# Optimization experiments

Hardware: AMD Instinct MI355X
Metric: run time of the kernel (lower is better)

Reference implementation:

```python
import jax, jax.numpy as jnp
import numpy as np

N = 50000       # nodes
E = 800000      # edges (before self-loops)
G = 512         # graphs in batch
IN_DIM = 128
OUT_DIM = 8
DIMS = [(IN_DIM, 32), (32, 64), (64, 128), (128, 64)]
EPS = 1e-5


def setup_inputs() -> dict:
    key = jax.random.key(0)
    ks = jax.random.split(key, 40)
    def nrm(k, shape, s=0.05):
        return jax.random.normal(k, shape, jnp.float32) * s
    inp = {}
    inp["x"] = jax.random.normal(ks[0], (N, IN_DIM), jnp.float32)
    inp["edge_index"] = jax.random.randint(ks[1], (2, E), 0, N, dtype=jnp.int32)
    inp["batch"] = jnp.sort(jax.random.randint(ks[2], (N,), 0, G, dtype=jnp.int32))
    for i, (din, dout) in enumerate(DIMS, 1):
        inp[f"W{i}"]  = nrm(ks[3 * i + 0], (din, dout))
        inp[f"as{i}"] = nrm(ks[3 * i + 1], (dout,))
        inp[f"ad{i}"] = nrm(ks[3 * i + 2], (dout,))
        inp[f"b{i}"]  = jnp.zeros((dout,), jnp.float32)
        inp[f"g{i}"]  = jnp.ones((dout,), jnp.float32)   # BN gamma
        inp[f"be{i}"] = jnp.zeros((dout,), jnp.float32)  # BN beta
    inp["Wf"] = nrm(ks[20], (64, 32)); inp["bf"] = jnp.zeros((32,), jnp.float32)
    inp["Wc"] = nrm(ks[21], (32, OUT_DIM)); inp["bc"] = jnp.zeros((OUT_DIM,), jnp.float32)
    return inp


def gat_conv(x, src, dst, W, a_s, a_d, b):
    """PyG GATConv, heads=1: linear (no bias) -> per-edge attention with
    leaky_relu(0.2) -> segment softmax over incoming edges -> scatter-add -> bias."""
    h = x @ W                                   # [N, F]
    a_src = h @ a_s                             # [N]
    a_dst = h @ a_d                             # [N]
    e = jax.nn.leaky_relu(a_src[src] + a_dst[dst], 0.2)   # [E+N]
    m = jax.ops.segment_max(e, dst, num_segments=N)
    w = jnp.exp(e - m[dst])
    denom = jax.ops.segment_sum(w, dst, num_segments=N)
    alpha = w / denom[dst]                      # self-loops guarantee denom > 0
    out = jax.ops.segment_sum(alpha[:, None] * h[src], dst, num_segments=N)
    return out + b


def batch_norm(x, g, be):
    mu = x.mean(axis=0)
    var = x.var(axis=0)                         # biased, as torch training BN
    return (x - mu) * jax.lax.rsqrt(var + EPS) * g + be


def reference(x, edge_index, batch,
              W1, as1, ad1, b1, g1, be1,
              W2, as2, ad2, b2, g2, be2,
              W3, as3, ad3, b3, g3, be3,
              W4, as4, ad4, b4, g4, be4,
              Wf, bf, Wc, bc):
    loops = jnp.arange(N, dtype=edge_index.dtype)
    src = jnp.concatenate([edge_index[0], loops])   # GATConv adds self-loops
    dst = jnp.concatenate([edge_index[1], loops])
    params = [(W1, as1, ad1, b1, g1, be1), (W2, as2, ad2, b2, g2, be2),
              (W3, as3, ad3, b3, g3, be3), (W4, as4, ad4, b4, g4, be4)]
    h = x
    for (W, a_s, a_d, b, g, be) in params:
        h = jax.nn.leaky_relu(gat_conv(h, src, dst, W, a_s, a_d, b), 0.01)
        h = batch_norm(h, g, be)
    pooled = jax.ops.segment_sum(h, batch, num_segments=G)   # global_add_pool
    z = jax.nn.leaky_relu(pooled @ Wf + bf, 0.01)
    return jax.nn.sigmoid(z @ Wc + bc)
```

## Files before the change

### kernel.cpp

```cpp
#include <hip/hip_runtime.h>
#include <math.h>

constexpr int BLK = 256;
constexpr int NBLKA = 256;

static inline int cdiv(long a, long b) { return (int)((a + b - 1) / b); }

typedef __attribute__((ext_vector_type(8))) short short8;
typedef __attribute__((ext_vector_type(4))) float floatx4;

__device__ __forceinline__ unsigned short f2bf(float f) {
    unsigned u = __float_as_uint(f);
    unsigned r = u + 0x7fffu + ((u >> 16) & 1u);
    return (unsigned short)(r >> 16);
}
__device__ __forceinline__ float bf2f(unsigned short s) {
    return __uint_as_float(((unsigned)s) << 16);
}


__global__ void histA_k(const int* __restrict__ dst, int* __restrict__ histg,
                        int E, int nbkt, int chunk) {
    __shared__ int h[256];
    int tid = threadIdx.x, z = blockIdx.x;
    h[tid] = 0;
    __syncthreads();
    int e0 = z * chunk, e1 = min(E, e0 + chunk);
    for (int e = e0 + tid; e < e1; e += BLK) atomicAdd(&h[dst[e] >> 8], 1);
    __syncthreads();
    if (tid < nbkt) histg[z * nbkt + tid] = h[tid];
}

__global__ void bucket_scan_k(const int* __restrict__ histg, int* __restrict__ bucket_base,
                              int nbkt, int E, int* __restrict__ gs, int* __restrict__ ge,
                              int G, float* __restrict__ bnstats) {
    __shared__ int s[BLK];
    int t = threadIdx.x;
    int v = 0;
    if (t < nbkt)
        for (int z = 0; z < NBLKA; ++z) v += histg[z * nbkt + t];
    s[t] = v;
    __syncthreads();
    for (int o = 1; o < BLK; o <<= 1) {
        int tv = (t >= o) ? s[t - o] : 0;
        __syncthreads();
        s[t] += tv;
        __syncthreads();
    }
    if (t < nbkt) bucket_base[t] = s[t] - v;
    if (t == 0) bucket_base[nbkt] = E;
    for (int i = t; i < G; i += BLK) { gs[i] = 0x7fffffff; ge[i] = -1; }
    for (int i = t; i < 1024; i += BLK) bnstats[i] = 0.f;
}

__global__ void blk_scan_k(int* __restrict__ histg, const int* __restrict__ bucket_base,
                           int nbkt) {
    __shared__ int s[BLK];
    int t = threadIdx.x, b = blockIdx.x;
    int v = histg[t * nbkt + b];
    s[t] = v;
    __syncthreads();
    for (int o = 1; o < BLK; o <<= 1) {
        int tv = (t >= o) ? s[t - o] : 0;
        __syncthreads();
        s[t] += tv;
        __syncthreads();
    }
    histg[t * nbkt + b] = bucket_base[b] + s[t] - v;
}

__global__ void scatterA_k(const int* __restrict__ src, const int* __restrict__ dst,
                           const int* __restrict__ histg, unsigned* __restrict__ ebkt,
                           int E, int nbkt, int chunk) {
    __shared__ int cur[256];
    int tid = threadIdx.x, z = blockIdx.x;
    if (tid < nbkt) cur[tid] = histg[z * nbkt + tid];
    __syncthreads();
    int e0 = z * chunk, e1 = min(E, e0 + chunk);
    for (int e = e0 + tid; e < e1; e += BLK) {
        int d = dst[e];
        int b = d >> 8;
        int pos = atomicAdd(&cur[b], 1);
        ebkt[pos] = ((unsigned)(d & 255) << 16) | (unsigned)src[e];
    }
}

__global__ void csrB_k(const unsigned* __restrict__ ebkt, const int* __restrict__ bucket_base,
                       int* __restrict__ off, unsigned short* __restrict__ csr,
                       const int* __restrict__ batch, int* __restrict__ gs,
                       int* __restrict__ ge, int N, int E, int nbkt) {
    __shared__ int dg[256];
    __shared__ int sc[256];
    int t = threadIdx.x, b = blockIdx.x;
    int n0 = b << 8;
    int cnt = min(256, N - n0);
    dg[t] = (t < cnt) ? 1 : 0;
    __syncthreads();
    int e0 = bucket_base[b], e1 = bucket_base[b + 1];
    for (int e = e0 + t; e < e1; e += BLK) atomicAdd(&dg[ebkt[e] >> 16], 1);
    __syncthreads();
    int d = dg[t];
    sc[t] = d;
    __syncthreads();
    for (int o = 1; o < BLK; o <<= 1) {
        int tv = (t >= o) ? sc[t - o] : 0;
        __syncthreads();
        sc[t] += tv;
        __syncthreads();
    }
    int loff = sc[t] - d;
    int csrbase = e0 + n0;
    if (t < cnt) {
        off[n0 + t] = csrbase + loff;
        csr[csrbase + loff] = (unsigned short)(n0 + t);
        dg[t] = loff + 1;
    }
    if (b == nbkt - 1 && t == 0) off[N] = E + N;
    int n = n0 + t;
    if (n < N) {
        int bb = batch[n];
        if (n == 0) gs[bb] = 0;
        else {
            int pb = batch[n - 1];
            if (pb != bb) { gs[bb] = n; ge[pb] = n - 1; }
        }
        if (n == N - 1) ge[bb] = N - 1;
    }
    __syncthreads();
    for (int e = e0 + t; e < e1; e += BLK) {
        unsigned w = ebkt[e];
        int pos = atomicAdd(&dg[w >> 16], 1);
        csr[csrbase + pos] = (unsigned short)(w & 0xffff);
    }
}

template <int K, int NOUT, bool AFP32, bool HASBN>
__launch_bounds__(256)
__global__ void gemm_fused(const void* __restrict__ av, const float* __restrict__ W,
                           const float* __restrict__ a_s, const float* __restrict__ a_d,
                           const float* __restrict__ bnst, const float* __restrict__ g_prev,
                           const float* __restrict__ be_prev, float invN,
                           unsigned short* __restrict__ hb,
                           float* __restrict__ asrc, float* __restrict__ adst, int N) {
    constexpr int KF = K / 32;
    __shared__ float s_sca[K], s_scc[K], s_rs[K], s_rd[K], s_bd[2];
    int tid = threadIdx.x;
    if (tid < K) {
        float a = 1.f, c = 0.f;
        if (HASBN) {
            float mu = bnst[tid] * invN;
            float var = bnst[128 + tid] * invN - mu * mu;
            a = g_prev[tid] * rsqrtf(var + 1e-5f);
            c = be_prev[tid] - mu * a;
        }
        s_sca[tid] = a; s_scc[tid] = c;
    }
    __syncthreads();
    const bool dots = (blockIdx.y == 0);
    if (dots) {
        if (tid < K) {
            const float* wr = W + (long)tid * NOUT;
            float rs = 0.f, rd = 0.f;
            for (int f = 0; f < NOUT; ++f) {
                float w = wr[f];
                rs += w * a_s[f];
                rd += w * a_d[f];
            }
            s_rs[tid] = rs; s_rd[tid] = rd;
        }
        __syncthreads();
        if (tid < 2) {
            const float* r = tid ? s_rd : s_rs;
            float b = 0.f;
            for (int k = 0; k < K; ++k) b += s_scc[k] * r[k];
            s_bd[tid] = b;
        }
        __syncthreads();
    }

    int wave = tid >> 6;
    int lane = tid & 63;
    int quad = lane >> 4;
    int r16 = lane & 15;
    int col = blockIdx.y * 16 + r16;

    short8 bfr[KF];
    float biasp = 0.f;
#pragma unroll
    for (int kk = 0; kk < KF; ++kk) {
        short8 b;
#pragma unroll
        for (int j = 0; j < 8; ++j) {
            int k = kk * 32 + quad * 8 + j;
            float w = W[(long)k * NOUT + col];
            b[j] = (short)f2bf(s_sca[k] * w);
            biasp += s_scc[k] * w;
        }
        bfr[kk] = b;
    }
    biasp += __shfl_xor(biasp, 16, 64);
    biasp += __shfl_xor(biasp, 32, 64);

    int blockbase = blockIdx.x * 128;
#pragma unroll
    for (int rt = 0; rt < 2; ++rt) {
        int tilebase = blockbase + wave * 32 + rt * 16;
        if (tilebase >= N) break;
        int arow = min(tilebase + r16, N - 1);
        short8 afr[KF];
        if (AFP32) {
            const float* xr = (const float*)av + (long)arow * K;
#pragma unroll
            for (int kk = 0; kk < KF; ++kk) {
                float4 x0 = *(const float4*)(xr + kk * 32 + quad * 8);
                float4 x1 = *(const float4*)(xr + kk * 32 + quad * 8 + 4);
                short8 a;
                a[0] = (short)f2bf(x0.x); a[1] = (short)f2bf(x0.y);
                a[2] = (short)f2bf(x0.z); a[3] = (short)f2bf(x0.w);
                a[4] = (short)f2bf(x1.x); a[5] = (short)f2bf(x1.y);
                a[6] = (short)f2bf(x1.z); a[7] = (short)f2bf(x1.w);
                afr[kk] = a;
            }
        } else {
            const unsigned short* hr = (const unsigned short*)av + (long)arow * K;
#pragma unroll
            for (int kk = 0; kk < KF; ++kk)
                afr[kk] = *(const short8*)(hr + kk * 32 + quad * 8);
        }
        floatx4 acc = {0.f, 0.f, 0.f, 0.f};
#pragma unroll
        for (int kk = 0; kk < KF; ++kk)
            acc = __builtin_amdgcn_mfma_f32_16x16x32_bf16(afr[kk], bfr[kk], acc, 0, 0, 0);
#pragma unroll
        for (int rr = 0; rr < 4; ++rr) {
            int srow = tilebase + quad * 4 + rr;
            if (srow < N) hb[(long)srow * NOUT + col] = f2bf(acc[rr] + biasp);
        }
        if (dots) {
            float ds = 0.f, dd = 0.f;
#pragma unroll
            for (int kk = 0; kk < KF; ++kk) {
                int kb = kk * 32 + quad * 8;
#pragma unroll
                for (int j = 0; j < 8; ++j) {
                    int k = kb + j;
                    float a = bf2f((unsigned short)afr[kk][j]) * s_sca[k];
                    ds += a * s_rs[k];
                    dd += a * s_rd[k];
                }
            }
            ds += __shfl_xor(ds, 16, 64); ds += __shfl_xor(ds, 32, 64);
            dd += __shfl_xor(dd, 16, 64); dd += __shfl_xor(dd, 32, 64);
            int drow = tilebase + r16;
            if (quad == 0 && drow < N) {
                asrc[drow] = ds + s_bd[0];
                adst[drow] = dd + s_bd[1];
            }
        }
    }
}

template <int DOUT>
__global__ void gather_fused(const int* __restrict__ off,
                             const unsigned short* __restrict__ csr,
                             const float* __restrict__ asrc, const float* __restrict__ adst,
                             const unsigned short* __restrict__ hb,
                             const float* __restrict__ b,
                             unsigned short* __restrict__ out, int N) {
    constexpr int TPN = DOUT / 8;
    int t = blockIdx.x * blockDim.x + threadIdx.x;
    int d = t / TPN;
    if (d >= N) return;
    int l = t % TPN;
    int p0 = off[d], p1 = off[d + 1];
    float ad = adst[d];
    const int f0 = l * 8;

    float acc[8];
#pragma unroll
    for (int i = 0; i < 8; ++i) acc[i] = 0.f;
    float sum = 0.f;

#pragma unroll 2
    for (int p = p0; p < p1; ++p) {
        int s = csr[p];
        float e = asrc[s] + ad;
        e = e > 0.f ? e : 0.2f * e;
        float w = __expf(e);
        sum += w;
        const uint4 hv = *(const uint4*)(hb + (long)s * DOUT + f0);
        acc[0] += w * bf2f((unsigned short)(hv.x & 0xffff));
        acc[1] += w * bf2f((unsigned short)(hv.x >> 16));
        acc[2] += w * bf2f((unsigned short)(hv.y & 0xffff));
        acc[3] += w * bf2f((unsigned short)(hv.y >> 16));
        acc[4] += w * bf2f((unsigned short)(hv.z & 0xffff));
        acc[5] += w * bf2f((unsigned short)(hv.z >> 16));
        acc[6] += w * bf2f((unsigned short)(hv.w & 0xffff));
        acc[7] += w * bf2f((unsigned short)(hv.w >> 16));
    }
    float inv = 1.f / sum;

    float4 b0 = *(const float4*)(b + f0);
    float4 b1 = *(const float4*)(b + f0 + 4);
    float bb[8] = {b0.x, b0.y, b0.z, b0.w, b1.x, b1.y, b1.z, b1.w};
    ushort4 o0, o1;
#pragma unroll
    for (int i = 0; i < 8; ++i) {
        float v = acc[i] * inv + bb[i];
        v = v > 0.f ? v : 0.01f * v;
        unsigned short hv = f2bf(v);
        if (i < 4) ((unsigned short*)&o0)[i] = hv;
        else       ((unsigned short*)&o1)[i - 4] = hv;
    }
    *(ushort4*)(out + (long)d * DOUT + f0) = o0;
    *(ushort4*)(out + (long)d * DOUT + f0 + 4) = o1;
}

template <int DOUT>
__global__ void stats_k(const unsigned short* __restrict__ y, float* __restrict__ bnsum,
                        float* __restrict__ bnsq, int N) {
    constexpr int QPR = DOUT / 8;
    __shared__ float ssum[DOUT];
    __shared__ float ssq[DOUT];
    for (int i = threadIdx.x; i < DOUT; i += blockDim.x) { ssum[i] = 0.f; ssq[i] = 0.f; }
    __syncthreads();
    long total = (long)N * QPR;
    long stride = (long)gridDim.x * blockDim.x;
    long t0 = (long)blockIdx.x * blockDim.x + threadIdx.x;
    int f0 = (int)(t0 % QPR) * 8;
    float ls[8], lq[8];
#pragma unroll
    for (int i = 0; i < 8; ++i) { ls[i] = 0.f; lq[i] = 0.f; }
    for (long t = t0; t < total; t += stride) {
        uint4 hv = *(const uint4*)(y + t * 8);
        unsigned vv[4] = {hv.x, hv.y, hv.z, hv.w};
#pragma unroll
        for (int q = 0; q < 4; ++q) {
            float v0 = bf2f((unsigned short)(vv[q] & 0xffff));
            float v1 = bf2f((unsigned short)(vv[q] >> 16));
            ls[2 * q] += v0;     lq[2 * q] += v0 * v0;
            ls[2 * q + 1] += v1; lq[2 * q + 1] += v1 * v1;
        }
    }
#pragma unroll
    for (int i = 0; i < 8; ++i) {
        atomicAdd(&ssum[f0 + i], ls[i]);
        atomicAdd(&ssq[f0 + i], lq[i]);
    }
    __syncthreads();
    for (int i = threadIdx.x; i < DOUT; i += blockDim.x) {
        atomicAdd(&bnsum[i], ssum[i]);
        atomicAdd(&bnsq[i], ssq[i]);
    }
}

__global__ void pool_head_k(const unsigned short* __restrict__ h, const int* __restrict__ gs,
                            const int* __restrict__ ge, const float* __restrict__ bnst,
                            const float* __restrict__ g4, const float* __restrict__ be4,
                            float invN, const float* __restrict__ Wf,
                            const float* __restrict__ bf, const float* __restrict__ Wc,
                            const float* __restrict__ bc, float* __restrict__ out) {
    int g = blockIdx.x;
    int t = threadIdx.x;
    __shared__ float p[64];
    __shared__ float z[32];
    float mu = bnst[t] * invN;
    float var = bnst[128 + t] * invN - mu * mu;
    float a = g4[t] * rsqrtf(var + 1e-5f);
    float c = be4[t] - mu * a;
    int s0 = gs[g], s1 = ge[g];
    float acc = 0.f, cnt = 0.f;
    if (s0 <= s1) {
        cnt = (float)(s1 - s0 + 1);
        for (int n = s0; n <= s1; ++n) acc += bf2f(h[(long)n * 64 + t]);
    }
    p[t] = a * acc + cnt * c;
    __syncthreads();
    if (t < 32) {
        float zacc = bf[t];
#pragma unroll
        for (int f = 0; f < 64; ++f) zacc += p[f] * Wf[f * 32 + t];
        z[t] = zacc > 0.f ? zacc : 0.01f * zacc;
    }
    __syncthreads();
    if (t < 8) {
        float oacc = bc[t];
#pragma unroll
        for (int o = 0; o < 32; ++o) oacc += z[o] * Wc[o * 8 + t];
        out[(long)g * 8 + t] = 1.f / (1.f + __expf(-oacc));
    }
}

extern "C" void kernel_launch(void* const* d_in, const int* in_sizes, int n_in,
                              void* d_out, int out_size, void* d_ws, size_t ws_size,
                              hipStream_t stream) {
    const float* x   = (const float*)d_in[0];
    const int* ei    = (const int*)d_in[1];
    const int* batch = (const int*)d_in[2];
    const int N  = in_sizes[2];
    const int E  = in_sizes[1] / 2;
    const int ET = E + N;
    const int G  = out_size / 8;
    const int* src = ei;
    const int* dst = ei + E;

    const float *W[4], *as_[4], *ad_[4], *bb[4], *gg[4], *be_[4];
    for (int i = 0; i < 4; ++i) {
        W[i]   = (const float*)d_in[3 + 6 * i];
        as_[i] = (const float*)d_in[4 + 6 * i];
        ad_[i] = (const float*)d_in[5 + 6 * i];
        bb[i]  = (const float*)d_in[6 + 6 * i];
        gg[i]  = (const float*)d_in[7 + 6 * i];
        be_[i] = (const float*)d_in[8 + 6 * i];
    }
    const float* Wf = (const float*)d_in[27];
    const float* bfp = (const float*)d_in[28];
    const float* Wc = (const float*)d_in[29];
    const float* bc = (const float*)d_in[30];

    float* ws = (float*)d_ws;
    long off_ = 0;
    auto alloc = [&](long nelem) { float* p = ws + off_; off_ += (nelem + 3) & ~3L; return p; };
    unsigned short* h2a = (unsigned short*)alloc((long)N * 64);
    unsigned short* h2b = (unsigned short*)alloc((long)N * 64);
    unsigned short* hb  = (unsigned short*)alloc((long)N * 64);
    float* asrc     = alloc(N);
    float* adst     = alloc(N);
    float* bnstats  = alloc(4 * 256);
    unsigned* ebkt  = (unsigned*)alloc(E);
    int* histg      = (int*)alloc((long)NBLKA * 256);
    int* bucket_base = (int*)alloc(260);
    int* off        = (int*)alloc(N + 1);
    unsigned short* csr = (unsigned short*)alloc(ET / 2 + 2);
    int* gs         = (int*)alloc(G);
    int* ge         = (int*)alloc(G);
    (void)ws_size; (void)n_in;

    const int nbkt = cdiv(N, 256);
    const int chunk = cdiv(E, NBLKA);
    const float invN = 1.f / (float)N;

    histA_k<<<NBLKA, BLK, 0, stream>>>(dst, histg, E, nbkt, chunk);
    bucket_scan_k<<<1, BLK, 0, stream>>>(histg, bucket_base, nbkt, E, gs, ge, G, bnstats);
    blk_scan_k<<<nbkt, BLK, 0, stream>>>(histg, bucket_base, nbkt);
    scatterA_k<<<NBLKA, BLK, 0, stream>>>(src, dst, histg, ebkt, E, nbkt, chunk);
    csrB_k<<<nbkt, BLK, 0, stream>>>(ebkt, bucket_base, off, csr, batch, gs, ge, N, E, nbkt);

#define LAYER(i, DIN, DOUT, AFP32, HASBN, INP, OUTP, BNPREV, GPREV, BEPREV)               \
    do {                                                                                  \
        gemm_fused<DIN, DOUT, AFP32, HASBN>                                               \
            <<<dim3(cdiv(N, 128), DOUT / 16), 256, 0, stream>>>(                          \
                INP, W[i], as_[i], ad_[i], BNPREV, GPREV, BEPREV, invN,                   \
                hb, asrc, adst, N);                                                       \
        gather_fused<DOUT><<<cdiv((long)N * (DOUT / 8), BLK), BLK, 0, stream>>>(          \
            off, csr, asrc, adst, hb, bb[i], OUTP, N);                                    \
        stats_k<DOUT><<<120, BLK, 0, stream>>>(OUTP, bnstats + i * 256,                   \
                                               bnstats + i * 256 + 128, N);               \
    } while (0)

    LAYER(0, 128, 32, true, false, x, h2b, bnstats, gg[0], be_[0]);
    LAYER(1, 32, 64, false, true, h2b, h2a, bnstats + 0 * 256, gg[0], be_[0]);
    LAYER(2, 64, 128, false, true, h2a, h2b, bnstats + 1 * 256, gg[1], be_[1]);
    LAYER(3, 128, 64, false, true, h2b, h2a, bnstats + 2 * 256, gg[2], be_[2]);
#undef LAYER

    pool_head_k<<<G, 64, 0, stream>>>(h2a, gs, ge, bnstats + 3 * 256, gg[3], be_[3],
                                      invN, Wf, bfp, Wc, bc, (float*)d_out);
}
```

Before: 375.5 us.

## Compute all GEMM column tiles per block, stripe BN stats, parallelize pooling

Result: faster. 355.5 us (-5.3%).

```diff
diff --git a/kernel.cpp b/kernel.cpp
--- a/kernel.cpp
+++ b/kernel.cpp
@@ -50,7 +50,7 @@
     if (t < nbkt) bucket_base[t] = s[t] - v;
     if (t == 0) bucket_base[nbkt] = E;
     for (int i = t; i < G; i += BLK) { gs[i] = 0x7fffffff; ge[i] = -1; }
-    for (int i = t; i < 1024; i += BLK) bnstats[i] = 0.f;
+    for (int i = t; i < 8192; i += BLK) bnstats[i] = 0.f;
 }
 
 __global__ void blk_scan_k(int* __restrict__ histg, const int* __restrict__ bucket_base,
@@ -143,21 +143,27 @@
                            unsigned short* __restrict__ hb,
                            float* __restrict__ asrc, float* __restrict__ adst, int N) {
     constexpr int KF = K / 32;
+    constexpr int NY = NOUT / 16;
     __shared__ float s_sca[K], s_scc[K], s_rs[K], s_rd[K], s_bd[2];
     int tid = threadIdx.x;
     if (tid < K) {
         float a = 1.f, c = 0.f;
         if (HASBN) {
-            float mu = bnst[tid] * invN;
-            float var = bnst[128 + tid] * invN - mu * mu;
+            float su = 0.f, sq = 0.f;
+#pragma unroll
+            for (int s = 0; s < 8; ++s) {
+                su += bnst[s * 256 + tid];
+                sq += bnst[s * 256 + 128 + tid];
+            }
+            float mu = su * invN;
+            float var = sq * invN - mu * mu;
             a = g_prev[tid] * rsqrtf(var + 1e-5f);
             c = be_prev[tid] - mu * a;
         }
         s_sca[tid] = a; s_scc[tid] = c;
     }
     __syncthreads();
-    const bool dots = (blockIdx.y == 0);
-    if (dots) {
+    {
         if (tid < K) {
             const float* wr = W + (long)tid * NOUT;
             float rs = 0.f, rd = 0.f;
@@ -182,32 +188,16 @@
     int lane = tid & 63;
     int quad = lane >> 4;
     int r16 = lane & 15;
-    int col = blockIdx.y * 16 + r16;
-
-    short8 bfr[KF];
-    float biasp = 0.f;
-#pragma unroll
-    for (int kk = 0; kk < KF; ++kk) {
-        short8 b;
-#pragma unroll
-        for (int j = 0; j < 8; ++j) {
-            int k = kk * 32 + quad * 8 + j;
-            float w = W[(long)k * NOUT + col];
-            b[j] = (short)f2bf(s_sca[k] * w);
-            biasp += s_scc[k] * w;
-        }
-        bfr[kk] = b;
-    }
-    biasp += __shfl_xor(biasp, 16, 64);
-    biasp += __shfl_xor(biasp, 32, 64);
-
     int blockbase = blockIdx.x * 128;
+
+    short8 afr[2][KF];
+    bool valid[2];
 #pragma unroll
     for (int rt = 0; rt < 2; ++rt) {
         int tilebase = blockbase + wave * 32 + rt * 16;
-        if (tilebase >= N) break;
+        valid[rt] = tilebase < N;
+        if (!valid[rt]) continue;
         int arow = min(tilebase + r16, N - 1);
-        short8 afr[KF];
         if (AFP32) {
             const float* xr = (const float*)av + (long)arow * K;
 #pragma unroll
@@ -219,42 +209,67 @@
                 a[2] = (short)f2bf(x0.z); a[3] = (short)f2bf(x0.w);
                 a[4] = (short)f2bf(x1.x); a[5] = (short)f2bf(x1.y);
                 a[6] = (short)f2bf(x1.z); a[7] = (short)f2bf(x1.w);
-                afr[kk] = a;
+                afr[rt][kk] = a;
             }
         } else {
             const unsigned short* hr = (const unsigned short*)av + (long)arow * K;
 #pragma unroll
             for (int kk = 0; kk < KF; ++kk)
-                afr[kk] = *(const short8*)(hr + kk * 32 + quad * 8);
-        }
-        floatx4 acc = {0.f, 0.f, 0.f, 0.f};
-#pragma unroll
-        for (int kk = 0; kk < KF; ++kk)
-            acc = __builtin_amdgcn_mfma_f32_16x16x32_bf16(afr[kk], bfr[kk], acc, 0, 0, 0);
-#pragma unroll
-        for (int rr = 0; rr < 4; ++rr) {
-            int srow = tilebase + quad * 4 + rr;
-            if (srow < N) hb[(long)srow * NOUT + col] = f2bf(acc[rr] + biasp);
-        }
-        if (dots) {
-            float ds = 0.f, dd = 0.f;
-#pragma unroll
-            for (int kk = 0; kk < KF; ++kk) {
-                int kb = kk * 32 + quad * 8;
-#pragma unroll
-                for (int j = 0; j < 8; ++j) {
-                    int k = kb + j;
-                    float a = bf2f((unsigned short)afr[kk][j]) * s_sca[k];
-                    ds += a * s_rs[k];
-                    dd += a * s_rd[k];
-                }
-            }
-            ds += __shfl_xor(ds, 16, 64); ds += __shfl_xor(ds, 32, 64);
-            dd += __shfl_xor(dd, 16, 64); dd += __shfl_xor(dd, 32, 64);
-            int drow = tilebase + r16;
-            if (quad == 0 && drow < N) {
-                asrc[drow] = ds + s_bd[0];
-                adst[drow] = dd + s_bd[1];
+                afr[rt][kk] = *(const short8*)(hr + kk * 32 + quad * 8);
+        }
+        float ds = 0.f, dd = 0.f;
+#pragma unroll
+        for (int kk = 0; kk < KF; ++kk) {
+            int kb = kk * 32 + quad * 8;
+#pragma unroll
+            for (int j = 0; j < 8; ++j) {
+                int k = kb + j;
+                float a = bf2f((unsigned short)afr[rt][kk][j]) * s_sca[k];
+                ds += a * s_rs[k];
+                dd += a * s_rd[k];
+            }
+        }
+        ds += __shfl_xor(ds, 16, 64); ds += __shfl_xor(ds, 32, 64);
+        dd += __shfl_xor(dd, 16, 64); dd += __shfl_xor(dd, 32, 64);
+        int drow = tilebase + r16;
+        if (quad == 0 && drow < N) {
+            asrc[drow] = ds + s_bd[0];
+            adst[drow] = dd + s_bd[1];
+        }
+    }
+
+#pragma unroll
+    for (int y = 0; y < NY; ++y) {
+        int col = y * 16 + r16;
+        short8 bfr[KF];
+        float biasp = 0.f;
+#pragma unroll
+        for (int kk = 0; kk < KF; ++kk) {
+            short8 b;
+#pragma unroll
+            for (int j = 0; j < 8; ++j) {
+                int k = kk * 32 + quad * 8 + j;
+                float w = W[(long)k * NOUT + col];
+                b[j] = (short)f2bf(s_sca[k] * w);
+                biasp += s_scc[k] * w;
+            }
+            bfr[kk] = b;
+        }
+        biasp += __shfl_xor(biasp, 16, 64);
+        biasp += __shfl_xor(biasp, 32, 64);
+
+#pragma unroll
+        for (int rt = 0; rt < 2; ++rt) {
+            if (!valid[rt]) continue;
+            int tilebase = blockbase + wave * 32 + rt * 16;
+            floatx4 acc = {0.f, 0.f, 0.f, 0.f};
+#pragma unroll
+            for (int kk = 0; kk < KF; ++kk)
+                acc = __builtin_amdgcn_mfma_f32_16x16x32_bf16(afr[rt][kk], bfr[kk], acc, 0, 0, 0);
+#pragma unroll
+            for (int rr = 0; rr < 4; ++rr) {
+                int srow = tilebase + quad * 4 + rr;
+                if (srow < N) hb[(long)srow * NOUT + col] = f2bf(acc[rr] + biasp);
             }
         }
     }
@@ -317,8 +332,7 @@
 }
 
 template <int DOUT>
-__global__ void stats_k(const unsigned short* __restrict__ y, float* __restrict__ bnsum,
-                        float* __restrict__ bnsq, int N) {
+__global__ void stats_k(const unsigned short* __restrict__ y, float* __restrict__ bn, int N) {
     constexpr int QPR = DOUT / 8;
     __shared__ float ssum[DOUT];
     __shared__ float ssq[DOUT];
@@ -348,9 +362,10 @@
         atomicAdd(&ssq[f0 + i], lq[i]);
     }
     __syncthreads();
+    float* base = bn + (blockIdx.x & 7) * 256;
     for (int i = threadIdx.x; i < DOUT; i += blockDim.x) {
-        atomicAdd(&bnsum[i], ssum[i]);
-        atomicAdd(&bnsq[i], ssq[i]);
+        atomicAdd(&base[i], ssum[i]);
+        atomicAdd(&base[128 + i], ssq[i]);
     }
 }
 
@@ -362,24 +377,35 @@
                             const float* __restrict__ bc, float* __restrict__ out) {
     int g = blockIdx.x;
     int t = threadIdx.x;
+    int f = t & 63, sub = t >> 6;
+    __shared__ float pp[4][64];
     __shared__ float p[64];
     __shared__ float z[32];
-    float mu = bnst[t] * invN;
-    float var = bnst[128 + t] * invN - mu * mu;
-    float a = g4[t] * rsqrtf(var + 1e-5f);
-    float c = be4[t] - mu * a;
     int s0 = gs[g], s1 = ge[g];
-    float acc = 0.f, cnt = 0.f;
-    if (s0 <= s1) {
-        cnt = (float)(s1 - s0 + 1);
-        for (int n = s0; n <= s1; ++n) acc += bf2f(h[(long)n * 64 + t]);
-    }
-    p[t] = a * acc + cnt * c;
+    float acc = 0.f;
+    if (s0 <= s1)
+        for (int n = s0 + sub; n <= s1; n += 4) acc += bf2f(h[(long)n * 64 + f]);
+    pp[sub][f] = acc;
+    __syncthreads();
+    if (t < 64) {
+        float su = 0.f, sq = 0.f;
+#pragma unroll
+        for (int s = 0; s < 8; ++s) {
+            su += bnst[s * 256 + t];
+            sq += bnst[s * 256 + 128 + t];
+        }
+        float mu = su * invN;
+        float var = sq * invN - mu * mu;
+        float a = g4[t] * rsqrtf(var + 1e-5f);
+        float c = be4[t] - mu * a;
+        float cnt = (s0 <= s1) ? (float)(s1 - s0 + 1) : 0.f;
+        p[t] = a * (pp[0][t] + pp[1][t] + pp[2][t] + pp[3][t]) + cnt * c;
+    }
     __syncthreads();
     if (t < 32) {
         float zacc = bf[t];
 #pragma unroll
-        for (int f = 0; f < 64; ++f) zacc += p[f] * Wf[f * 32 + t];
+        for (int ff = 0; ff < 64; ++ff) zacc += p[ff] * Wf[ff * 32 + t];
         z[t] = zacc > 0.f ? zacc : 0.01f * zacc;
     }
     __syncthreads();
@@ -426,7 +452,7 @@
     unsigned short* hb  = (unsigned short*)alloc((long)N * 64);
     float* asrc     = alloc(N);
     float* adst     = alloc(N);
-    float* bnstats  = alloc(4 * 256);
+    float* bnstats  = alloc(4 * 2048);
     unsigned* ebkt  = (unsigned*)alloc(E);
     int* histg      = (int*)alloc((long)NBLKA * 256);
     int* bucket_base = (int*)alloc(260);
@@ -449,21 +475,20 @@
 #define LAYER(i, DIN, DOUT, AFP32, HASBN, INP, OUTP, BNPREV, GPREV, BEPREV)               \
     do {                                                                                  \
         gemm_fused<DIN, DOUT, AFP32, HASBN>                                               \
-            <<<dim3(cdiv(N, 128), DOUT / 16), 256, 0, stream>>>(                          \
+            <<<cdiv(N, 128), 256, 0, stream>>>(                                           \
                 INP, W[i], as_[i], ad_[i], BNPREV, GPREV, BEPREV, invN,                   \
                 hb, asrc, adst, N);                                                       \
         gather_fused<DOUT><<<cdiv((long)N * (DOUT / 8), BLK), BLK, 0, stream>>>(          \
             off, csr, asrc, adst, hb, bb[i], OUTP, N);                                    \
-        stats_k<DOUT><<<120, BLK, 0, stream>>>(OUTP, bnstats + i * 256,                   \
-                                               bnstats + i * 256 + 128, N);               \
+        stats_k<DOUT><<<240, BLK, 0, stream>>>(OUTP, bnstats + i * 2048, N);              \
     } while (0)
 
     LAYER(0, 128, 32, true, false, x, h2b, bnstats, gg[0], be_[0]);
-    LAYER(1, 32, 64, false, true, h2b, h2a, bnstats + 0 * 256, gg[0], be_[0]);
-    LAYER(2, 64, 128, false, true, h2a, h2b, bnstats + 1 * 256, gg[1], be_[1]);
-    LAYER(3, 128, 64, false, true, h2b, h2a, bnstats + 2 * 256, gg[2], be_[2]);
+    LAYER(1, 32, 64, false, true, h2b, h2a, bnstats + 0 * 2048, gg[0], be_[0]);
+    LAYER(2, 64, 128, false, true, h2a, h2b, bnstats + 1 * 2048, gg[1], be_[1]);
+    LAYER(3, 128, 64, false, true, h2b, h2a, bnstats + 2 * 2048, gg[2], be_[2]);
 #undef LAYER
 
-    pool_head_k<<<G, 64, 0, stream>>>(h2a, gs, ge, bnstats + 3 * 256, gg[3], be_[3],
-                                      invN, Wf, bfp, Wc, bc, (float*)d_out);
-}
+    pool_head_k<<<G, 256, 0, stream>>>(h2a, gs, ge, bnstats + 3 * 2048, gg[3], be_[3],
+                                       invN, Wf, bfp, Wc, bc, (float*)d_out);
+}
```
